# Performance work log

Measured on AMD Instinct MI355X. Metric: run time of the kernel, lower is better.

Reference implementation:

```python
import jax, jax.numpy as jnp
import numpy as np

N, E, R = 30000, 300000, 3
IN, HID, OUT, HEADS = 256, 32, 64, 4
NEG_SLOPE = 0.2  # DGL GATConv default


def setup_inputs() -> dict:
    key = jax.random.key(0)
    ks = jax.random.split(key, 10)
    x = jax.random.normal(ks[0], (N, IN), jnp.float32)
    src = jax.random.randint(ks[1], (R, E), 0, N)
    dst = jax.random.randint(ks[2], (R, E), 0, N)
    s1 = (2.0 / IN) ** 0.5
    W1 = jax.random.normal(ks[3], (R, IN, HEADS * HID), jnp.float32) * s1
    attn_l1 = jax.random.normal(ks[4], (R, HEADS, HID), jnp.float32) * 0.1
    attn_r1 = jax.random.normal(ks[5], (R, HEADS, HID), jnp.float32) * 0.1
    b1 = jnp.zeros((R, HEADS * HID), jnp.float32)
    s2 = (2.0 / (HEADS * HID)) ** 0.5
    W2 = jax.random.normal(ks[6], (R, HEADS * HID, HEADS * OUT), jnp.float32) * s2
    attn_l2 = jax.random.normal(ks[7], (R, HEADS, OUT), jnp.float32) * 0.1
    attn_r2 = jax.random.normal(ks[8], (R, HEADS, OUT), jnp.float32) * 0.1
    b2 = jnp.zeros((R, HEADS * OUT), jnp.float32)
    return dict(x=x, src=src, dst=dst, W1=W1, attn_l1=attn_l1, attn_r1=attn_r1,
                b1=b1, W2=W2, attn_l2=attn_l2, attn_r2=attn_r2, b2=b2)


def _gat(x, s, d, W, al, ar, b):
    """Single-relation GATConv (DGL semantics): gather, edge softmax, scatter."""
    n = x.shape[0]
    H, D = al.shape
    z = (x @ W).reshape(n, H, D)                 # [n,H,D]
    el = (z * al[None]).sum(-1)                  # [n,H]
    er = (z * ar[None]).sum(-1)                  # [n,H]
    e = jax.nn.leaky_relu(el[s] + er[d], NEG_SLOPE)   # [E,H]
    m = jax.ops.segment_max(e, d, num_segments=n)     # stable edge softmax per dst
    w = jnp.exp(e - m[d])
    denom = jax.ops.segment_sum(w, d, num_segments=n)
    alpha = w / denom[d]                         # [E,H]
    out = jax.ops.segment_sum(alpha[:, :, None] * z[s], d, num_segments=n)  # [n,H,D]
    return out + b.reshape(1, H, D)


def reference(x, src, dst, W1, attn_l1, attn_r1, b1, W2, attn_l2, attn_r2, b2):
    gat_r = jax.vmap(_gat, in_axes=(None, 0, 0, 0, 0, 0, 0))
    # conv1: per-relation GAT summed across relations (HeteroGraphConv aggregate='sum')
    h = gat_r(x, src, dst, W1, attn_l1, attn_r1, b1).sum(0)      # [N,HEADS,HID]
    h = jax.nn.relu(h).reshape(-1, HEADS * HID)                  # [N,HEADS*HID]
    # conv2
    h2 = gat_r(h, src, dst, W2, attn_l2, attn_r2, b2).sum(0)     # [N,HEADS,OUT]
    return h2.mean(axis=1)                                       # [N,OUT]
```

## Files before the change

kernel.cpp:

```cpp
#include <hip/hip_runtime.h>
#include <math.h>

#define NNODES 30000
#define MPAD   30080
#define NEDGES 300000
#define NREL 3
#define IND 256
#define HIDD 32
#define OUTD 64
#define NHEADS 4
#define C1 (NHEADS*HIDD)
#define C2 (NHEADS*OUTD)
#define NEG_SLOPE 0.2f
#define CAP 64

typedef short bf16x8 __attribute__((ext_vector_type(8)));
typedef float f32x4  __attribute__((ext_vector_type(4)));

__device__ __forceinline__ float b2f(unsigned short u) {
    return __uint_as_float(((unsigned)u) << 16);
}
__device__ __forceinline__ unsigned short f2b(float f) {
    unsigned u = __float_as_uint(f);
    u += 0x7fffu + ((u >> 16) & 1u);
    return (unsigned short)(u >> 16);
}

template<int K, int N>
__device__ __forceinline__ void pack_w_dev(const float* __restrict__ W,
                                           unsigned short* __restrict__ P, int t) {
    const int KS = K / 32, NT = N / 16;
    int lane = t & 63;
    int fid = t >> 6;
    if (fid >= NREL * NT * KS) return;
    int ks = fid % KS;
    int nt = (fid / KS) % NT;
    int r  = fid / (KS * NT);
    int n  = nt * 16 + (lane & 15);
    int k0 = ks * 32 + (lane >> 4) * 8;
    const float* Wr = W + (size_t)r * K * N;
    unsigned short o[8];
#pragma unroll
    for (int j = 0; j < 8; j++) o[j] = f2b(Wr[(size_t)(k0 + j) * N + n]);
    unsigned short* dst = P + (size_t)fid * 512 + lane * 8;
    *(ushort4*)&dst[0] = *(ushort4*)&o[0];
    *(ushort4*)&dst[4] = *(ushort4*)&o[4];
}

__device__ __forceinline__ void pack_v_dev(const float* __restrict__ W2,
                                           unsigned short* __restrict__ P, int t) {
    const int KS = 16, NT = 4;
    int lane = t & 63;
    int fid = t >> 6;
    if (fid >= NREL * NT * KS) return;
    int ks = fid % KS;
    int nt = (fid / KS) % NT;
    int r  = fid / (KS * NT);
    int n  = nt * 16 + (lane & 15);
    int k0 = ks * 32 + (lane >> 4) * 8;
    const float* Wr = W2 + (size_t)r * C1 * C2;
    unsigned short o[8];
#pragma unroll
    for (int j = 0; j < 8; j++) {
        int k = k0 + j;
        int c = k & 127, h = k >> 7;
        o[j] = f2b(Wr[(size_t)c * C2 + h * OUTD + n]);
    }
    unsigned short* dst = P + (size_t)fid * 512 + lane * 8;
    *(ushort4*)&dst[0] = *(ushort4*)&o[0];
    *(ushort4*)&dst[4] = *(ushort4*)&o[4];
}

#define CAST_BLOCKS (NNODES * IND / 4 / 256)
#define PACK1_BLOCKS (NREL * (C1/16) * (IND/32) / 4)
#define PACKV_BLOCKS (NREL * 4 * 16 / 4)
#define VLR_BLOCKS 6
#define PREP_BLOCKS (CAST_BLOCKS + PACK1_BLOCKS + PACKV_BLOCKS + VLR_BLOCKS + 1)
__global__ void prep_kernel(const float* __restrict__ x, unsigned short* __restrict__ Xh,
                            const float* __restrict__ W1, unsigned short* __restrict__ P1,
                            const float* __restrict__ W2, unsigned short* __restrict__ PV,
                            const float* __restrict__ al2, const float* __restrict__ ar2,
                            const float* __restrict__ bb2,
                            float* __restrict__ tabs, float* __restrict__ biasout) {
    int b = blockIdx.x;
    if (b < CAST_BLOCKS) {
        int i = (b * 256 + threadIdx.x) * 4;
        float4 v = *(const float4*)&x[i];
        ushort4 o = { f2b(v.x), f2b(v.y), f2b(v.z), f2b(v.w) };
        *(ushort4*)&Xh[i] = o;
    } else if (b < CAST_BLOCKS + PACK1_BLOCKS) {
        pack_w_dev<IND, C1>(W1, P1, (b - CAST_BLOCKS) * 256 + threadIdx.x);
    } else if (b < CAST_BLOCKS + PACK1_BLOCKS + PACKV_BLOCKS) {
        pack_v_dev(W2, PV, (b - CAST_BLOCKS - PACK1_BLOCKS) * 256 + threadIdx.x);
    } else if (b < CAST_BLOCKS + PACK1_BLOCKS + PACKV_BLOCKS + VLR_BLOCKS) {
        int t = (b - CAST_BLOCKS - PACK1_BLOCKS - PACKV_BLOCKS) * 256 + threadIdx.x;
        if (t < NREL * NHEADS * C1) {
            int c = t & 127, rh = t >> 7;
            const float* Wr = W2 + (size_t)(rh >> 2) * C1 * C2 + (size_t)c * C2 + (rh & 3) * OUTD;
            const float* alp = al2 + (size_t)rh * OUTD;
            const float* arp = ar2 + (size_t)rh * OUTD;
            float sl = 0.f, sr = 0.f;
#pragma unroll 4
            for (int d = 0; d < OUTD; d++) {
                sl = fmaf(Wr[d], alp[d], sl);
                sr = fmaf(Wr[d], arp[d], sr);
            }
            tabs[(rh * 2 + 0) * C1 + c] = sl;
            tabs[(rh * 2 + 1) * C1 + c] = sr;
        }
    } else {
        int t = threadIdx.x;
        if (t < OUTD) {
            float s = 0.f;
#pragma unroll
            for (int rh = 0; rh < NREL * NHEADS; rh++)
                s += bb2[(size_t)(rh >> 2) * C2 + (rh & 3) * OUTD + t];
            biasout[t] = 0.25f * s;
        }
    }
}

template<int K, int N>
__global__ __launch_bounds__(256) void mfma_gemm(
    const unsigned short* __restrict__ Ah, const unsigned short* __restrict__ Bp,
    const float* __restrict__ al, const float* __restrict__ ar,
    unsigned short* __restrict__ Zh, float* __restrict__ el, float* __restrict__ er)
{
    const int KS = K / 32, NT = N / 16, MT = 64, NP = N + 4;
    const int wave = threadIdx.x >> 6, lane = threadIdx.x & 63;
    const int r  = blockIdx.y;
    const int m0 = blockIdx.x * MT;
    const int fcol = lane & 15, quad = lane >> 4;

    __shared__ unsigned short zs[MT * (N + 4)];

    int m = m0 + wave * 16 + fcol;
    if (m >= NNODES) m = NNODES - 1;
    bf16x8 afrag[KS];
    const unsigned short* arow = Ah + (size_t)m * K + quad * 8;
#pragma unroll
    for (int ks = 0; ks < KS; ks++) afrag[ks] = *(const bf16x8*)(arow + ks * 32);

    f32x4 acc[NT];
#pragma unroll
    for (int nt = 0; nt < NT; nt++) { f32x4 z = {0.f,0.f,0.f,0.f}; acc[nt] = z; }

    const unsigned short* Bpr = Bp + (size_t)r * NT * KS * 512;
    for (int ks = 0; ks < KS; ks++) {
        bf16x8 b[NT];
#pragma unroll
        for (int nt = 0; nt < NT; nt++)
            b[nt] = *(const bf16x8*)(Bpr + ((size_t)nt * KS + ks) * 512 + lane * 8);
#pragma unroll
        for (int nt = 0; nt < NT; nt++)
            acc[nt] = __builtin_amdgcn_mfma_f32_16x16x32_bf16(afrag[ks], b[nt], acc[nt], 0, 0, 0);
    }

    {
        int lrow = wave * 16 + quad * 4;
#pragma unroll
        for (int nt = 0; nt < NT; nt++)
#pragma unroll
            for (int q = 0; q < 4; q++)
                zs[(lrow + q) * NP + nt * 16 + fcol] = f2b(acc[nt][q]);
    }
    __syncthreads();

    {
        uint2* zo = (uint2*)(Zh + ((size_t)r * MPAD + m0) * N);
        for (int i = threadIdx.x; i < MT * N / 4; i += 256) {
            int row = i / (N / 4), c4 = i % (N / 4);
            zo[i] = *(const uint2*)&zs[row * NP + c4 * 4];
        }
    }
    {
        const int D = N / NHEADS;
        int row = threadIdx.x >> 2, h = threadIdx.x & 3;
        int n = m0 + row;
        if (n < NNODES) {
            const float* alp = al + ((size_t)r * NHEADS + h) * D;
            const float* arp = ar + ((size_t)r * NHEADS + h) * D;
            const unsigned short* zp = zs + row * NP + h * D;
            float sl = 0.f, sr = 0.f;
#pragma unroll
            for (int d0 = 0; d0 < D; d0 += 4) {
                uint2 u = *(const uint2*)&zp[d0];
                float z0 = b2f((unsigned short)(u.x & 0xffff));
                float z1 = b2f((unsigned short)(u.x >> 16));
                float z2 = b2f((unsigned short)(u.y & 0xffff));
                float z3 = b2f((unsigned short)(u.y >> 16));
                sl = fmaf(z0, alp[d0], sl);     sr = fmaf(z0, arp[d0], sr);
                sl = fmaf(z1, alp[d0 + 1], sl); sr = fmaf(z1, arp[d0 + 1], sr);
                sl = fmaf(z2, alp[d0 + 2], sl); sr = fmaf(z2, arp[d0 + 2], sr);
                sl = fmaf(z3, alp[d0 + 3], sl); sr = fmaf(z3, arp[d0 + 3], sr);
            }
            el[((size_t)r * NNODES + n) * NHEADS + h] = sl;
            er[((size_t)r * NNODES + n) * NHEADS + h] = sr;
        }
    }
}

__global__ void bucket_fill(const int* __restrict__ src, const int* __restrict__ dst,
                            unsigned* __restrict__ cnt, int* __restrict__ buck) {
    int gid = blockIdx.x * blockDim.x + threadIdx.x;
    if (gid >= NREL * NEDGES) return;
    int r = gid / NEDGES;
    int d = dst[gid];
    int base = r * NNODES + d;
    unsigned pos = atomicAdd(&cnt[base], 1u);
    if (pos < CAP) buck[(size_t)base * CAP + pos] = src[gid];
}

__device__ __forceinline__ float wave_max(float t) {
#pragma unroll
    for (int o = 1; o < 64; o <<= 1) t = fmaxf(t, __shfl_xor(t, o, 64));
    return t;
}
__device__ __forceinline__ float wave_sum(float t) {
#pragma unroll
    for (int o = 1; o < 64; o <<= 1) t += __shfl_xor(t, o, 64);
    return t;
}

__global__ __launch_bounds__(256) void gat_gather1(
    const unsigned* __restrict__ cnt, const int* __restrict__ buck,
    const float* __restrict__ el, const float* __restrict__ er,
    const unsigned short* __restrict__ Zh, const float* __restrict__ b1,
    unsigned short* __restrict__ hbh)
{
    __shared__ float atab[4][4 * 65];
    int wave = threadIdx.x >> 6, lane = threadIdx.x & 63;
    int n = blockIdx.x * 4 + wave;
    if (n >= NNODES) return;
    const int h0 = lane >> 4;
    float accx = 0.f, accy = 0.f;
    for (int r = 0; r < NREL; r++) {
        int base = r * NNODES + n;
        int c = (int)cnt[base]; c = c < CAP ? c : CAP;
        if (c == 0) continue;
        int s_lane = (lane < c) ? buck[(size_t)base * CAP + lane] : -1;
        float lg[4];
        if (s_lane >= 0) {
            const float4 e4 = *(const float4*)&el[((size_t)r * NNODES + s_lane) * NHEADS];
            const float4 r4 = *(const float4*)&er[(size_t)base * NHEADS];
            float v;
            v = e4.x + r4.x; lg[0] = v > 0.f ? v : NEG_SLOPE * v;
            v = e4.y + r4.y; lg[1] = v > 0.f ? v : NEG_SLOPE * v;
            v = e4.z + r4.z; lg[2] = v > 0.f ? v : NEG_SLOPE * v;
            v = e4.w + r4.w; lg[3] = v > 0.f ? v : NEG_SLOPE * v;
        } else {
            lg[0] = lg[1] = lg[2] = lg[3] = -INFINITY;
        }
#pragma unroll
        for (int h = 0; h < 4; h++) {
            float m = wave_max(lg[h]);
            float w = (lane < c) ? __expf(lg[h] - m) : 0.f;
            float den = wave_sum(w);
            atab[wave][h * 65 + lane] = w / den;
        }
        const unsigned short* Zr = Zh + (size_t)r * MPAD * C1;
        const float* at = atab[wave] + h0 * 65;
        int j = 0;
        for (; j + 3 < c; j += 4) {
            int s0 = __builtin_amdgcn_readlane(s_lane, j);
            int s1 = __builtin_amdgcn_readlane(s_lane, j + 1);
            int s2 = __builtin_amdgcn_readlane(s_lane, j + 2);
            int s3 = __builtin_amdgcn_readlane(s_lane, j + 3);
            const ushort2 za = *(const ushort2*)&Zr[(size_t)s0 * C1 + 2 * lane];
            const ushort2 zb = *(const ushort2*)&Zr[(size_t)s1 * C1 + 2 * lane];
            const ushort2 zc = *(const ushort2*)&Zr[(size_t)s2 * C1 + 2 * lane];
            const ushort2 zd = *(const ushort2*)&Zr[(size_t)s3 * C1 + 2 * lane];
            float a0 = at[j], a1 = at[j + 1], a2 = at[j + 2], a3 = at[j + 3];
            accx = fmaf(a0, b2f(za.x), accx); accy = fmaf(a0, b2f(za.y), accy);
            accx = fmaf(a1, b2f(zb.x), accx); accy = fmaf(a1, b2f(zb.y), accy);
            accx = fmaf(a2, b2f(zc.x), accx); accy = fmaf(a2, b2f(zc.y), accy);
            accx = fmaf(a3, b2f(zd.x), accx); accy = fmaf(a3, b2f(zd.y), accy);
        }
        for (; j < c; j++) {
            int s = __builtin_amdgcn_readlane(s_lane, j);
            float a0 = at[j];
            const ushort2 z2 = *(const ushort2*)&Zr[(size_t)s * C1 + 2 * lane];
            accx = fmaf(a0, b2f(z2.x), accx);
            accy = fmaf(a0, b2f(z2.y), accy);
        }
    }
    int cch = 2 * lane;
    float bx = b1[cch]     + b1[C1 + cch]     + b1[2 * C1 + cch];
    float by = b1[cch + 1] + b1[C1 + cch + 1] + b1[2 * C1 + cch + 1];
    ushort2 o;
    o.x = f2b(fmaxf(accx + bx, 0.f));
    o.y = f2b(fmaxf(accy + by, 0.f));
    *(ushort2*)&hbh[(size_t)n * C1 + cch] = o;
}

__global__ __launch_bounds__(256) void elr2_kernel(
    const unsigned short* __restrict__ hbh, const float* __restrict__ tabs,
    float* __restrict__ el, float* __restrict__ er)
{
    int wave = threadIdx.x >> 6, lane = threadIdx.x & 63;
    int n = blockIdx.x * 4 + wave;
    unsigned z = *(const unsigned*)&hbh[(size_t)n * C1 + 2 * lane];
    float z0 = __uint_as_float(z << 16);
    float z1 = __uint_as_float(z & 0xffff0000u);
    float p[24];
#pragma unroll
    for (int j = 0; j < 24; j++) {
        float2 t = *(const float2*)&tabs[j * C1 + 2 * lane];
        p[j] = fmaf(z1, t.y, z0 * t.x);
    }
#pragma unroll
    for (int o = 1; o < 64; o <<= 1) {
#pragma unroll
        for (int j = 0; j < 24; j++) p[j] += __shfl_xor(p[j], o, 64);
    }
    if (lane == 0) {
#pragma unroll
        for (int j = 0; j < 24; j++) {
            int rh = j >> 1;
            size_t idx = ((size_t)(rh >> 2) * NNODES + n) * NHEADS + (rh & 3);
            if (j & 1) er[idx] = p[j]; else el[idx] = p[j];
        }
    }
}

__global__ __launch_bounds__(1024, 8) void gat_gather2f(
    const unsigned* __restrict__ cnt, const int* __restrict__ buck,
    const float* __restrict__ el, const float* __restrict__ er,
    const unsigned short* __restrict__ hbh, const unsigned short* __restrict__ PV,
    const float* __restrict__ biasout, float* __restrict__ out)
{
    __shared__ unsigned short aggs[16 * 1536];
    __shared__ float atv[16][64 * 4];
    const int wave = threadIdx.x >> 6, lane = threadIdx.x & 63;
    const int fcol = lane & 15, quad = lane >> 4;
    const int n0 = blockIdx.x * 16;
    const int n  = n0 + wave;

    for (int r = 0; r < NREL; r++) {
        float ag[8];
#pragma unroll
        for (int k = 0; k < 8; k++) ag[k] = 0.f;

        int base = r * NNODES + n;
        int c = (int)cnt[base]; c = c < CAP ? c : CAP;
        if (c > 0) {
            int s_lane = (lane < c) ? buck[(size_t)base * CAP + lane] : -1;
            float lg[4];
            if (s_lane >= 0) {
                const float4 e4 = *(const float4*)&el[((size_t)r * NNODES + s_lane) * NHEADS];
                const float4 r4 = *(const float4*)&er[(size_t)base * NHEADS];
                float v;
                v = e4.x + r4.x; lg[0] = v > 0.f ? v : NEG_SLOPE * v;
                v = e4.y + r4.y; lg[1] = v > 0.f ? v : NEG_SLOPE * v;
                v = e4.z + r4.z; lg[2] = v > 0.f ? v : NEG_SLOPE * v;
                v = e4.w + r4.w; lg[3] = v > 0.f ? v : NEG_SLOPE * v;
            } else {
                lg[0] = lg[1] = lg[2] = lg[3] = -INFINITY;
            }
            float aw[4];
#pragma unroll
            for (int h = 0; h < 4; h++) {
                float m = wave_max(lg[h]);
                float w = (lane < c) ? __expf(lg[h] - m) : 0.f;
                float den = wave_sum(w);
                aw[h] = w / den;
            }
            float4 aq = { aw[0], aw[1], aw[2], aw[3] };
            *(float4*)&atv[wave][lane * 4] = aq;
            const float4* at = (const float4*)&atv[wave][0];

#define EDGE1(zz, aa)                                                           \
            {   float z0 = __uint_as_float((zz) << 16);                         \
                float z1 = __uint_as_float((zz) & 0xffff0000u);                 \
                ag[0] = fmaf((aa).x, z0, ag[0]); ag[1] = fmaf((aa).x, z1, ag[1]); \
                ag[2] = fmaf((aa).y, z0, ag[2]); ag[3] = fmaf((aa).y, z1, ag[3]); \
                ag[4] = fmaf((aa).z, z0, ag[4]); ag[5] = fmaf((aa).z, z1, ag[5]); \
                ag[6] = fmaf((aa).w, z0, ag[6]); ag[7] = fmaf((aa).w, z1, ag[7]); }
            int j = 0;
            for (; j + 3 < c; j += 4) {
                int s0 = __builtin_amdgcn_readlane(s_lane, j);
                int s1 = __builtin_amdgcn_readlane(s_lane, j + 1);
                int s2 = __builtin_amdgcn_readlane(s_lane, j + 2);
                int s3 = __builtin_amdgcn_readlane(s_lane, j + 3);
                unsigned za = *(const unsigned*)&hbh[(size_t)s0 * C1 + 2 * lane];
                unsigned zb = *(const unsigned*)&hbh[(size_t)s1 * C1 + 2 * lane];
                unsigned zc = *(const unsigned*)&hbh[(size_t)s2 * C1 + 2 * lane];
                unsigned zd = *(const unsigned*)&hbh[(size_t)s3 * C1 + 2 * lane];
                float4 a0 = at[j], a1 = at[j + 1], a2 = at[j + 2], a3 = at[j + 3];
                EDGE1(za, a0); EDGE1(zb, a1); EDGE1(zc, a2); EDGE1(zd, a3);
            }
            for (; j < c; j++) {
                int s = __builtin_amdgcn_readlane(s_lane, j);
                unsigned zz = *(const unsigned*)&hbh[(size_t)s * C1 + 2 * lane];
                float4 a0 = at[j];
                EDGE1(zz, a0);
            }
#undef EDGE1
        }

        {
            unsigned sw = (unsigned)((wave & 7) << 4);
            char* basep = (char*)aggs + wave * 3072 + r * 1024;
#pragma unroll
            for (int h = 0; h < 4; h++) {
                unsigned pk = ((unsigned)f2b(ag[2 * h + 1]) << 16) | f2b(ag[2 * h]);
                *(unsigned*)(basep + (((unsigned)(h * 256 + lane * 4)) ^ sw)) = pk;
            }
        }
    }

    __syncthreads();

    if (wave < 4) {
        f32x4 acc = {0.f, 0.f, 0.f, 0.f};
        for (int rr = 0; rr < NREL; rr++) {
            const unsigned short* PVr = PV + ((size_t)(rr * 4 + wave) * 16) * 512;
#pragma unroll
            for (int ks = 0; ks < 16; ks++) {
                bf16x8 b = *(const bf16x8*)(PVr + (size_t)ks * 512 + lane * 8);
                const char* ap = (const char*)aggs + fcol * 3072 +
                                 (((unsigned)(rr * 1024 + ks * 64 + quad * 16)) ^
                                  ((unsigned)((fcol & 7) << 4)));
                bf16x8 a = *(const bf16x8*)ap;
                acc = __builtin_amdgcn_mfma_f32_16x16x32_bf16(a, b, acc, 0, 0, 0);
            }
        }
        int col = wave * 16 + fcol;
        float bias = biasout[col];
#pragma unroll
        for (int q = 0; q < 4; q++) {
            int row = n0 + quad * 4 + q;
            out[(size_t)row * OUTD + col] = fmaf(0.25f, acc[q], bias);
        }
    }
}

extern "C" void kernel_launch(void* const* d_in, const int* in_sizes, int n_in,
                              void* d_out, int out_size, void* d_ws, size_t ws_size,
                              hipStream_t stream) {
    (void)in_sizes; (void)n_in; (void)out_size; (void)ws_size;
    const float* x   = (const float*)d_in[0];
    const int*   src = (const int*)d_in[1];
    const int*   dst = (const int*)d_in[2];
    const float* W1  = (const float*)d_in[3];
    const float* al1 = (const float*)d_in[4];
    const float* ar1 = (const float*)d_in[5];
    const float* b1  = (const float*)d_in[6];
    const float* W2  = (const float*)d_in[7];
    const float* al2 = (const float*)d_in[8];
    const float* ar2 = (const float*)d_in[9];
    const float* b2  = (const float*)d_in[10];
    float* out = (float*)d_out;

    float* ws = (float*)d_ws;
    size_t off = 0;
    unsigned short* Zh  = (unsigned short*)(ws + off); off += (size_t)NREL * MPAD * C2 / 2;
    unsigned short* Xh  = (unsigned short*)(ws + off); off += (size_t)NNODES * IND / 2;
    unsigned short* hbh = (unsigned short*)(ws + off); off += (size_t)NNODES * C1 / 2;
    unsigned short* P1  = (unsigned short*)(ws + off); off += (size_t)NREL * (C1/16) * (IND/32) * 512 / 2;
    unsigned short* PV  = (unsigned short*)(ws + off); off += (size_t)NREL * 4 * 16 * 512 / 2;
    float* el  = ws + off; off += (size_t)NREL * NNODES * NHEADS;
    float* er  = ws + off; off += (size_t)NREL * NNODES * NHEADS;
    unsigned* cnt = (unsigned*)(ws + off); off += (size_t)NREL * NNODES;
    int* buck  = (int*)(ws + off); off += (size_t)NREL * NNODES * CAP;
    float* tabs    = ws + off; off += 24 * C1;
    float* biasout = ws + off; off += OUTD;

    const int TB = 256;

    hipMemsetAsync(cnt, 0, (size_t)NREL * NNODES * sizeof(unsigned), stream);
    bucket_fill<<<(NREL * NEDGES + TB - 1) / TB, TB, 0, stream>>>(src, dst, cnt, buck);
    prep_kernel<<<PREP_BLOCKS, TB, 0, stream>>>(x, Xh, W1, P1, W2, PV, al2, ar2, b2,
                                                tabs, biasout);

    {
        dim3 grid(MPAD / 64, NREL);
        mfma_gemm<IND, C1><<<grid, 256, 0, stream>>>(Xh, P1, al1, ar1, Zh, el, er);
    }
    gat_gather1<<<(NNODES + 3) / 4, 256, 0, stream>>>(cnt, buck, el, er, Zh, b1, hbh);

    elr2_kernel<<<NNODES / 4, 256, 0, stream>>>(hbh, tabs, el, er);
    gat_gather2f<<<NNODES / 16, 1024, 0, stream>>>(cnt, buck, el, er, hbh, PV, biasout, out);
}
```

Before: 371.5 us.

## Fuse layer-2 attention logits into gather1, shrink gather2 blocks, pack FMAs

The separate elr2 kernel is folded into gat_gather1, which now computes the layer-2 el/er dot products right after writing each hidden row, saving one launch and a re-read of hbh. The results go to new el2/er2 buffers so layer-1 el/er are not overwritten while gather1 is still reading them. gat_gather2f is resized from 16 to 8 nodes per block (512 threads), with the MFMA reading 8 real rows, duplicating them into the unused rows and storing only half the output. Inner-loop accumulations use 2-wide vector FMAs so the compiler can emit packed FP32 instructions.

```diff
diff --git a/kernel.cpp b/kernel.cpp
--- a/kernel.cpp
+++ b/kernel.cpp
@@ -16,6 +16,7 @@
 
 typedef short bf16x8 __attribute__((ext_vector_type(8)));
 typedef float f32x4  __attribute__((ext_vector_type(4)));
+typedef float f32x2  __attribute__((ext_vector_type(2)));
 
 __device__ __forceinline__ float b2f(unsigned short u) {
     return __uint_as_float(((unsigned)u) << 16);
@@ -226,14 +227,15 @@
     const unsigned* __restrict__ cnt, const int* __restrict__ buck,
     const float* __restrict__ el, const float* __restrict__ er,
     const unsigned short* __restrict__ Zh, const float* __restrict__ b1,
-    unsigned short* __restrict__ hbh)
+    const float* __restrict__ tabs,
+    unsigned short* __restrict__ hbh, float* __restrict__ el2, float* __restrict__ er2)
 {
     __shared__ float atab[4][4 * 65];
     int wave = threadIdx.x >> 6, lane = threadIdx.x & 63;
     int n = blockIdx.x * 4 + wave;
     if (n >= NNODES) return;
     const int h0 = lane >> 4;
-    float accx = 0.f, accy = 0.f;
+    f32x2 acc2 = {0.f, 0.f};
     for (int r = 0; r < NREL; r++) {
         int base = r * NNODES + n;
         int c = (int)cnt[base]; c = c < CAP ? c : CAP;
@@ -260,86 +262,81 @@
         }
         const unsigned short* Zr = Zh + (size_t)r * MPAD * C1;
         const float* at = atab[wave] + h0 * 65;
+#define EDGE1A(uu, aa)                                                          \
+        {   f32x2 zv = { __uint_as_float((uu) << 16),                           \
+                         __uint_as_float((uu) & 0xffff0000u) };                 \
+            acc2 = __builtin_elementwise_fma((f32x2){(aa), (aa)}, zv, acc2); }
         int j = 0;
         for (; j + 3 < c; j += 4) {
             int s0 = __builtin_amdgcn_readlane(s_lane, j);
             int s1 = __builtin_amdgcn_readlane(s_lane, j + 1);
             int s2 = __builtin_amdgcn_readlane(s_lane, j + 2);
             int s3 = __builtin_amdgcn_readlane(s_lane, j + 3);
-            const ushort2 za = *(const ushort2*)&Zr[(size_t)s0 * C1 + 2 * lane];
-            const ushort2 zb = *(const ushort2*)&Zr[(size_t)s1 * C1 + 2 * lane];
-            const ushort2 zc = *(const ushort2*)&Zr[(size_t)s2 * C1 + 2 * lane];
-            const ushort2 zd = *(const ushort2*)&Zr[(size_t)s3 * C1 + 2 * lane];
+            unsigned za = *(const unsigned*)&Zr[(size_t)s0 * C1 + 2 * lane];
+            unsigned zb = *(const unsigned*)&Zr[(size_t)s1 * C1 + 2 * lane];
+            unsigned zc = *(const unsigned*)&Zr[(size_t)s2 * C1 + 2 * lane];
+            unsigned zd = *(const unsigned*)&Zr[(size_t)s3 * C1 + 2 * lane];
             float a0 = at[j], a1 = at[j + 1], a2 = at[j + 2], a3 = at[j + 3];
-            accx = fmaf(a0, b2f(za.x), accx); accy = fmaf(a0, b2f(za.y), accy);
-            accx = fmaf(a1, b2f(zb.x), accx); accy = fmaf(a1, b2f(zb.y), accy);
-            accx = fmaf(a2, b2f(zc.x), accx); accy = fmaf(a2, b2f(zc.y), accy);
-            accx = fmaf(a3, b2f(zd.x), accx); accy = fmaf(a3, b2f(zd.y), accy);
+            EDGE1A(za, a0); EDGE1A(zb, a1); EDGE1A(zc, a2); EDGE1A(zd, a3);
         }
         for (; j < c; j++) {
             int s = __builtin_amdgcn_readlane(s_lane, j);
             float a0 = at[j];
-            const ushort2 z2 = *(const ushort2*)&Zr[(size_t)s * C1 + 2 * lane];
-            accx = fmaf(a0, b2f(z2.x), accx);
-            accy = fmaf(a0, b2f(z2.y), accy);
-        }
+            unsigned zz = *(const unsigned*)&Zr[(size_t)s * C1 + 2 * lane];
+            EDGE1A(zz, a0);
+        }
+#undef EDGE1A
     }
     int cch = 2 * lane;
     float bx = b1[cch]     + b1[C1 + cch]     + b1[2 * C1 + cch];
     float by = b1[cch + 1] + b1[C1 + cch + 1] + b1[2 * C1 + cch + 1];
     ushort2 o;
-    o.x = f2b(fmaxf(accx + bx, 0.f));
-    o.y = f2b(fmaxf(accy + by, 0.f));
+    o.x = f2b(fmaxf(acc2.x + bx, 0.f));
+    o.y = f2b(fmaxf(acc2.y + by, 0.f));
     *(ushort2*)&hbh[(size_t)n * C1 + cch] = o;
-}
-
-__global__ __launch_bounds__(256) void elr2_kernel(
-    const unsigned short* __restrict__ hbh, const float* __restrict__ tabs,
-    float* __restrict__ el, float* __restrict__ er)
-{
-    int wave = threadIdx.x >> 6, lane = threadIdx.x & 63;
-    int n = blockIdx.x * 4 + wave;
-    unsigned z = *(const unsigned*)&hbh[(size_t)n * C1 + 2 * lane];
-    float z0 = __uint_as_float(z << 16);
-    float z1 = __uint_as_float(z & 0xffff0000u);
-    float p[24];
-#pragma unroll
-    for (int j = 0; j < 24; j++) {
-        float2 t = *(const float2*)&tabs[j * C1 + 2 * lane];
-        p[j] = fmaf(z1, t.y, z0 * t.x);
-    }
-#pragma unroll
-    for (int o = 1; o < 64; o <<= 1) {
-#pragma unroll
-        for (int j = 0; j < 24; j++) p[j] += __shfl_xor(p[j], o, 64);
-    }
-    if (lane == 0) {
-#pragma unroll
-        for (int j = 0; j < 24; j++) {
-            int rh = j >> 1;
-            size_t idx = ((size_t)(rh >> 2) * NNODES + n) * NHEADS + (rh & 3);
-            if (j & 1) er[idx] = p[j]; else el[idx] = p[j];
-        }
-    }
-}
-
-__global__ __launch_bounds__(1024, 8) void gat_gather2f(
+
+    float hx = b2f(o.x), hy = b2f(o.y);
+    for (int half = 0; half < 2; half++) {
+        float p[12];
+#pragma unroll
+        for (int j = 0; j < 12; j++) {
+            const float2 t = *(const float2*)&tabs[(half * 12 + j) * C1 + cch];
+            p[j] = fmaf(hy, t.y, hx * t.x);
+        }
+#pragma unroll
+        for (int o2 = 1; o2 < 64; o2 <<= 1) {
+#pragma unroll
+            for (int j = 0; j < 12; j++) p[j] += __shfl_xor(p[j], o2, 64);
+        }
+        if (lane == 0) {
+#pragma unroll
+            for (int j = 0; j < 12; j++) {
+                int jj = half * 12 + j;
+                int rh = jj >> 1;
+                size_t idx = ((size_t)(rh >> 2) * NNODES + n) * NHEADS + (rh & 3);
+                if (jj & 1) er2[idx] = p[j]; else el2[idx] = p[j];
+            }
+        }
+    }
+}
+
+__global__ __launch_bounds__(512, 8) void gat_gather2f(
     const unsigned* __restrict__ cnt, const int* __restrict__ buck,
     const float* __restrict__ el, const float* __restrict__ er,
     const unsigned short* __restrict__ hbh, const unsigned short* __restrict__ PV,
     const float* __restrict__ biasout, float* __restrict__ out)
 {
-    __shared__ unsigned short aggs[16 * 1536];
-    __shared__ float atv[16][64 * 4];
+    __shared__ unsigned short aggs[8 * 1536];
+    __shared__ float atv[8][64 * 4];
     const int wave = threadIdx.x >> 6, lane = threadIdx.x & 63;
     const int fcol = lane & 15, quad = lane >> 4;
-    const int n0 = blockIdx.x * 16;
+    const int n0 = blockIdx.x * 8;
     const int n  = n0 + wave;
 
     for (int r = 0; r < NREL; r++) {
-        float ag[8];
-#pragma unroll
-        for (int k = 0; k < 8; k++) ag[k] = 0.f;
+        f32x2 ag[4];
+#pragma unroll
+        for (int k = 0; k < 4; k++) ag[k] = (f32x2){0.f, 0.f};
 
         int base = r * NNODES + n;
         int c = (int)cnt[base]; c = c < CAP ? c : CAP;
@@ -369,13 +366,13 @@
             *(float4*)&atv[wave][lane * 4] = aq;
             const float4* at = (const float4*)&atv[wave][0];
 
-#define EDGE1(zz, aa)                                                           \
-            {   float z0 = __uint_as_float((zz) << 16);                         \
-                float z1 = __uint_as_float((zz) & 0xffff0000u);                 \
-                ag[0] = fmaf((aa).x, z0, ag[0]); ag[1] = fmaf((aa).x, z1, ag[1]); \
-                ag[2] = fmaf((aa).y, z0, ag[2]); ag[3] = fmaf((aa).y, z1, ag[3]); \
-                ag[4] = fmaf((aa).z, z0, ag[4]); ag[5] = fmaf((aa).z, z1, ag[5]); \
-                ag[6] = fmaf((aa).w, z0, ag[6]); ag[7] = fmaf((aa).w, z1, ag[7]); }
+#define EDGE1(zz, aa)                                                             \
+            {   f32x2 zv = { __uint_as_float((zz) << 16),                         \
+                             __uint_as_float((zz) & 0xffff0000u) };               \
+                ag[0] = __builtin_elementwise_fma((f32x2){(aa).x,(aa).x}, zv, ag[0]); \
+                ag[1] = __builtin_elementwise_fma((f32x2){(aa).y,(aa).y}, zv, ag[1]); \
+                ag[2] = __builtin_elementwise_fma((f32x2){(aa).z,(aa).z}, zv, ag[2]); \
+                ag[3] = __builtin_elementwise_fma((f32x2){(aa).w,(aa).w}, zv, ag[3]); }
             int j = 0;
             for (; j + 3 < c; j += 4) {
                 int s0 = __builtin_amdgcn_readlane(s_lane, j);
@@ -399,11 +396,11 @@
         }
 
         {
-            unsigned sw = (unsigned)((wave & 7) << 4);
+            unsigned sw = (unsigned)(wave << 4);
             char* basep = (char*)aggs + wave * 3072 + r * 1024;
 #pragma unroll
             for (int h = 0; h < 4; h++) {
-                unsigned pk = ((unsigned)f2b(ag[2 * h + 1]) << 16) | f2b(ag[2 * h]);
+                unsigned pk = ((unsigned)f2b(ag[h].y) << 16) | f2b(ag[h].x);
                 *(unsigned*)(basep + (((unsigned)(h * 256 + lane * 4)) ^ sw)) = pk;
             }
         }
@@ -413,24 +410,27 @@
 
     if (wave < 4) {
         f32x4 acc = {0.f, 0.f, 0.f, 0.f};
+        const int arow = fcol & 7;
         for (int rr = 0; rr < NREL; rr++) {
             const unsigned short* PVr = PV + ((size_t)(rr * 4 + wave) * 16) * 512;
 #pragma unroll
             for (int ks = 0; ks < 16; ks++) {
                 bf16x8 b = *(const bf16x8*)(PVr + (size_t)ks * 512 + lane * 8);
-                const char* ap = (const char*)aggs + fcol * 3072 +
+                const char* ap = (const char*)aggs + arow * 3072 +
                                  (((unsigned)(rr * 1024 + ks * 64 + quad * 16)) ^
-                                  ((unsigned)((fcol & 7) << 4)));
+                                  ((unsigned)(arow << 4)));
                 bf16x8 a = *(const bf16x8*)ap;
                 acc = __builtin_amdgcn_mfma_f32_16x16x32_bf16(a, b, acc, 0, 0, 0);
             }
         }
-        int col = wave * 16 + fcol;
-        float bias = biasout[col];
-#pragma unroll
-        for (int q = 0; q < 4; q++) {
-            int row = n0 + quad * 4 + q;
-            out[(size_t)row * OUTD + col] = fmaf(0.25f, acc[q], bias);
+        if (quad < 2) {
+            int col = wave * 16 + fcol;
+            float bias = biasout[col];
+#pragma unroll
+            for (int q = 0; q < 4; q++) {
+                int row = n0 + quad * 4 + q;
+                out[(size_t)row * OUTD + col] = fmaf(0.25f, acc[q], bias);
+            }
         }
     }
 }
@@ -454,13 +454,15 @@
 
     float* ws = (float*)d_ws;
     size_t off = 0;
-    unsigned short* Zh  = (unsigned short*)(ws + off); off += (size_t)NREL * MPAD * C2 / 2;
+    unsigned short* Zh  = (unsigned short*)(ws + off); off += (size_t)NREL * MPAD * C1 / 2;
     unsigned short* Xh  = (unsigned short*)(ws + off); off += (size_t)NNODES * IND / 2;
     unsigned short* hbh = (unsigned short*)(ws + off); off += (size_t)NNODES * C1 / 2;
     unsigned short* P1  = (unsigned short*)(ws + off); off += (size_t)NREL * (C1/16) * (IND/32) * 512 / 2;
     unsigned short* PV  = (unsigned short*)(ws + off); off += (size_t)NREL * 4 * 16 * 512 / 2;
     float* el  = ws + off; off += (size_t)NREL * NNODES * NHEADS;
     float* er  = ws + off; off += (size_t)NREL * NNODES * NHEADS;
+    float* el2 = ws + off; off += (size_t)NREL * NNODES * NHEADS;
+    float* er2 = ws + off; off += (size_t)NREL * NNODES * NHEADS;
     unsigned* cnt = (unsigned*)(ws + off); off += (size_t)NREL * NNODES;
     int* buck  = (int*)(ws + off); off += (size_t)NREL * NNODES * CAP;
     float* tabs    = ws + off; off += 24 * C1;
@@ -477,8 +479,8 @@
         dim3 grid(MPAD / 64, NREL);
         mfma_gemm<IND, C1><<<grid, 256, 0, stream>>>(Xh, P1, al1, ar1, Zh, el, er);
     }
-    gat_gather1<<<(NNODES + 3) / 4, 256, 0, stream>>>(cnt, buck, el, er, Zh, b1, hbh);
-
-    elr2_kernel<<<NNODES / 4, 256, 0, stream>>>(hbh, tabs, el, er);
-    gat_gather2f<<<NNODES / 16, 1024, 0, stream>>>(cnt, buck, el, er, hbh, PV, biasout, out);
-}
+    gat_gather1<<<(NNODES + 3) / 4, 256, 0, stream>>>(cnt, buck, el, er, Zh, b1, tabs,
+                                                      hbh, el2, er2);
+
+    gat_gather2f<<<NNODES / 8, 512, 0, stream>>>(cnt, buck, el2, er2, hbh, PV, biasout, out);
+}
```

After: 363.7 us. -2.1%, faster.
